# Optimization experiments

Hardware: AMD Instinct MI355X
Metric: run time of the kernel (lower is better)

The kernel has to match this reference:

```python
import jax, jax.numpy as jnp
import numpy as np
import math

B, T, C, H, E = 1, 384, 512, 8, 16
D = C // H

def layer_norm(x, w, b, eps=1e-5):
    mu = jnp.mean(x, axis=-1, keepdims=True)
    var = jnp.mean(jnp.square(x - mu), axis=-1, keepdims=True)
    return (x - mu) * jax.lax.rsqrt(var + eps) * w + b

def setup_inputs() -> dict:
    key = jax.random.key(0)
    ks = jax.random.split(key, 12)
    s = 0.02
    return {
        'x': jax.random.normal(ks[0], (B, T, C), jnp.float32),
        'bias_matrix': jax.random.randint(ks[1], (B, T, T), 0, E, jnp.int32),
        'ln1_w': jnp.ones((C,), jnp.float32),
        'ln1_b': jnp.zeros((C,), jnp.float32),
        'w_attn_w': jax.random.normal(ks[2], (3 * C, C), jnp.float32) * s,
        'w_attn_b': jnp.zeros((3 * C,), jnp.float32),
        'w_proj_w': jax.random.normal(ks[3], (C, C), jnp.float32) * s,
        'w_proj_b': jnp.zeros((C,), jnp.float32),
        'attn_bias_emb': jax.random.normal(ks[4], (E, H), jnp.float32) * s,
        'edge_emb': jax.random.normal(ks[5], (E, C), jnp.float32) * s,
        'w_edge_k_w': jax.random.normal(ks[6], (C, C), jnp.float32) * s,
        'w_edge_k_b': jnp.zeros((C,), jnp.float32),
        'w_edge_v_w': jax.random.normal(ks[7], (C, C), jnp.float32) * s,
        'w_edge_v_b': jnp.zeros((C,), jnp.float32),
        'ln2_w': jnp.ones((C,), jnp.float32),
        'ln2_b': jnp.zeros((C,), jnp.float32),
        'c_fc_w': jax.random.normal(ks[8], (4 * C, C), jnp.float32) * s,
        'c_fc_b': jnp.zeros((4 * C,), jnp.float32),
        'c_proj_w': jax.random.normal(ks[9], (C, 4 * C), jnp.float32) * s,
        'c_proj_b': jnp.zeros((C,), jnp.float32),
    }

def reference(x, bias_matrix, ln1_w, ln1_b, w_attn_w, w_attn_b, w_proj_w, w_proj_b,
              attn_bias_emb, edge_emb, w_edge_k_w, w_edge_k_b, w_edge_v_w, w_edge_v_b,
              ln2_w, ln2_b, c_fc_w, c_fc_b, c_proj_w, c_proj_b):
    # --- attention branch ---
    h = layer_norm(x, ln1_w, ln1_b)
    qkv = h @ w_attn_w.T + w_attn_b                      # (B,T,3C)
    q, k, v = jnp.split(qkv, 3, axis=-1)
    q = q.reshape(B, T, H, D).transpose(0, 2, 1, 3)      # (B,H,T,D)
    k = k.reshape(B, T, H, D).transpose(0, 2, 1, 3)
    v = v.reshape(B, T, H, D).transpose(0, 2, 1, 3)
    scale = math.sqrt(D)

    ee = edge_emb[bias_matrix]                           # (B,T,T,C)
    e_k = (ee @ w_edge_k_w.T + w_edge_k_b).reshape(B, T, T, H, D)
    # score[b,h,i,j] = sum_d q[b,h,i,d] * k[b,h,j,d] * e_k[b,i,j,h,d]
    scores = jnp.einsum('bhid,bhjd,bijhd->bhij', q, k, e_k) / scale

    mask = jnp.tril(jnp.ones((T, T), bool))              # causal, diag included
    scores = jnp.where(mask, scores, -jnp.inf)
    ab = attn_bias_emb[bias_matrix].transpose(0, 3, 1, 2)  # (B,H,T,T)
    ab = jnp.where(mask, ab, 0.0)
    attn = jax.nn.softmax(scores + ab, axis=-1)

    e_v = (ee @ w_edge_v_w.T + w_edge_v_b).reshape(B, T, T, H, D)
    # y[b,h,i,d] = sum_j attn[b,h,i,j] * v[b,h,j,d] * e_v[b,i,j,h,d]
    y = jnp.einsum('bhij,bhjd,bijhd->bhid', attn, v, e_v)
    y = y.transpose(0, 2, 1, 3).reshape(B, T, C)
    y = y @ w_proj_w.T + w_proj_b
    x = x + y

    # --- MLP branch ---
    h2 = layer_norm(x, ln2_w, ln2_b)
    h2 = jax.nn.gelu(h2 @ c_fc_w.T + c_fc_b, approximate=False)
    x = x + (h2 @ c_proj_w.T + c_proj_b)
    return x
```

## Files before the change

kernel.cpp:

```cpp
#include <hip/hip_runtime.h>
#include <math.h>

#define TT 384
#define CC 512
#define HH 8
#define EE 16

typedef __bf16 bf16_t;
typedef __bf16 bf16x8 __attribute__((ext_vector_type(8)));
typedef __bf16 bf16x4v __attribute__((ext_vector_type(4)));
typedef float f32x4 __attribute__((ext_vector_type(4)));

__device__ __forceinline__ float wave_reduce_sum(float v) {
#pragma unroll
  for (int off = 32; off >= 1; off >>= 1) v += __shfl_xor(v, off, 64);
  return v;
}

__device__ __forceinline__ void wrow_unit(const float* __restrict__ wr,
                                          const float* __restrict__ g,
                                          const float* __restrict__ bb,
                                          float extra_c, bf16_t* __restrict__ orow,
                                          float* __restrict__ s1p,
                                          float* __restrict__ cp, int lane) {
  const float* p = wr + lane * 8;
  f32x4 w0 = *(const f32x4*)p, w1 = *(const f32x4*)(p + 4);
  f32x4 g0 = *(const f32x4*)(g + lane * 8), g1 = *(const f32x4*)(g + lane * 8 + 4);
  f32x4 b0 = *(const f32x4*)(bb + lane * 8), b1 = *(const f32x4*)(bb + lane * 8 + 4);
  f32x4 p0 = w0 * g0, p1 = w1 * g1;
  bf16x8 o;
  o[0] = (bf16_t)p0.x; o[1] = (bf16_t)p0.y; o[2] = (bf16_t)p0.z; o[3] = (bf16_t)p0.w;
  o[4] = (bf16_t)p1.x; o[5] = (bf16_t)p1.y; o[6] = (bf16_t)p1.z; o[7] = (bf16_t)p1.w;
  *(bf16x8*)(orow + lane * 8) = o;
  float s1 = p0.x + p0.y + p0.z + p0.w + p1.x + p1.y + p1.z + p1.w;
  float c = w0.x * b0.x + w0.y * b0.y + w0.z * b0.z + w0.w * b0.w +
            w1.x * b1.x + w1.y * b1.y + w1.z * b1.z + w1.w * b1.w;
  s1 = wave_reduce_sum(s1);
  c = wave_reduce_sum(c);
  if (lane == 0) { *s1p = s1; *cp = c + extra_c; }
}

struct PrepX {
  const float *eemb, *wekw, *wekb, *wevw, *wevb;
  const float *ln2w, *ln2b, *cfcw, *cfcb;
  const float *wproj, *wcproj;
  float *ektab, *evtab, *s1f, *cf, *x1s1, *x1s2;
  bf16_t *wfc_bf, *wproj_bf, *wcproj_bf;
};

__device__ void prep_unit(int u, const PrepX& X, int tid) {
  int lane = tid & 63, wave = tid >> 6;
  if (u < 256) {
    int wid = u * 4 + wave;
    int gbase = wid * 16;
    int table = gbase >> 13;
    int e = (gbase >> 9) & 15;
    int c0 = gbase & 511;
    const float* er = X.eemb + e * 512 + lane * 8;
    f32x4 ea = *(const f32x4*)er;
    f32x4 eb = *(const f32x4*)(er + 4);
    const float* wbase = table ? X.wevw : X.wekw;
    const float* bbase = table ? X.wevb : X.wekb;
    float* obase = (table ? X.evtab : X.ektab) + e * 512;
#pragma unroll
    for (int o = 0; o < 16; o++) {
      int c = c0 + o;
      const float* wr = wbase + (size_t)c * 512 + lane * 8;
      f32x4 wa = *(const f32x4*)wr;
      f32x4 wb = *(const f32x4*)(wr + 4);
      float acc = ea.x * wa.x + ea.y * wa.y + ea.z * wa.z + ea.w * wa.w +
                  eb.x * wb.x + eb.y * wb.y + eb.z * wb.z + eb.w * wb.w;
      acc = wave_reduce_sum(acc);
      if (lane == 0) obase[c] = acc + bbase[c];
    }
  } else if (u < 768) {
    int n = (u - 256) * 4 + wave;
    wrow_unit(X.cfcw + (size_t)n * 512, X.ln2w, X.ln2b, X.cfcb[n],
              X.wfc_bf + (size_t)n * 512, X.s1f + n, X.cf + n, lane);
  } else if (u < 1024) {
    int base = (u - 768) * 1024;
    for (int t = tid; t < 1024; t += 256) {
      f32x4 a = *((const f32x4*)X.wcproj + base + t);
      bf16x4v o;
      o[0] = (bf16_t)a.x; o[1] = (bf16_t)a.y; o[2] = (bf16_t)a.z; o[3] = (bf16_t)a.w;
      *((bf16x4v*)X.wcproj_bf + base + t) = o;
    }
  } else if (u < 1088) {
    int base = (u - 1024) * 1024;
    for (int t = tid; t < 1024; t += 256) {
      f32x4 a = *((const f32x4*)X.wproj + base + t);
      bf16x4v o;
      o[0] = (bf16_t)a.x; o[1] = (bf16_t)a.y; o[2] = (bf16_t)a.z; o[3] = (bf16_t)a.w;
      *((bf16x4v*)X.wproj_bf + base + t) = o;
    }
  } else if (u == 1088) {
    for (int i = tid; i < 384; i += 256) { X.x1s1[i] = 0.f; X.x1s2[i] = 0.f; }
  }
}

__global__ __launch_bounds__(256) void qkv_k(
    const float* __restrict__ x, const float* __restrict__ wattn,
    const float* __restrict__ ln1w, const float* __restrict__ ln1b,
    const float* __restrict__ wattnb, bf16_t* __restrict__ out, PrepX X) {
  int tid = threadIdx.x;
  if (blockIdx.y >= 12) {
    prep_unit((blockIdx.y - 12) * gridDim.x + blockIdx.x, X, tid);
    return;
  }
  __shared__ float part[4][32][32];
  __shared__ float rst[2][4][32];
  __shared__ float wst[2][4][32];
  int lane = tid & 63, wave = tid >> 6;
  int m0 = blockIdx.y * 32, n0 = blockIdx.x * 32;
  int r16 = lane & 15, quad = lane >> 4;
  int k0 = wave * 128;

  f32x4 acc[2][2];
  f32x4 zero = {0.f, 0.f, 0.f, 0.f};
#pragma unroll
  for (int i = 0; i < 2; i++)
#pragma unroll
    for (int j = 0; j < 2; j++) acc[i][j] = zero;

  const float* Af = x + (size_t)(m0 + r16) * 512 + k0 + quad * 8;
  const float* Wf = wattn + (size_t)(n0 + r16) * 512 + k0 + quad * 8;
  const float* gp = ln1w + k0 + quad * 8;
  const float* bp = ln1b + k0 + quad * 8;

  float sx[2] = {0.f, 0.f}, sxx[2] = {0.f, 0.f};
  float s1[2] = {0.f, 0.f}, cc[2] = {0.f, 0.f};

  for (int kb0 = 0; kb0 < 128; kb0 += 64) {
    uint4 araw[2][2][2], wraw[2][2][2];
#pragma unroll
    for (int u = 0; u < 2; u++) {
      int kb = kb0 + u * 32;
#pragma unroll
      for (int t = 0; t < 2; t++) {
        araw[u][t][0] = *(const uint4*)(Af + (size_t)t * 16 * 512 + kb);
        araw[u][t][1] = *(const uint4*)(Af + (size_t)t * 16 * 512 + kb + 4);
        wraw[u][t][0] = *(const uint4*)(Wf + (size_t)t * 16 * 512 + kb);
        wraw[u][t][1] = *(const uint4*)(Wf + (size_t)t * 16 * 512 + kb + 4);
      }
    }
#pragma unroll
    for (int u = 0; u < 2; u++) {
      int kb = kb0 + u * 32;
      f32x4 g0 = *(const f32x4*)(gp + kb), g1 = *(const f32x4*)(gp + kb + 4);
      f32x4 b0 = *(const f32x4*)(bp + kb), b1 = *(const f32x4*)(bp + kb + 4);
      bf16x8 af[2], bfr[2];
#pragma unroll
      for (int t = 0; t < 2; t++) {
        f32x4 a0 = *reinterpret_cast<const f32x4*>(&araw[u][t][0]);
        f32x4 a1 = *reinterpret_cast<const f32x4*>(&araw[u][t][1]);
        af[t][0] = (bf16_t)a0.x; af[t][1] = (bf16_t)a0.y;
        af[t][2] = (bf16_t)a0.z; af[t][3] = (bf16_t)a0.w;
        af[t][4] = (bf16_t)a1.x; af[t][5] = (bf16_t)a1.y;
        af[t][6] = (bf16_t)a1.z; af[t][7] = (bf16_t)a1.w;
        sx[t] += a0.x + a0.y + a0.z + a0.w + a1.x + a1.y + a1.z + a1.w;
        sxx[t] += a0.x * a0.x + a0.y * a0.y + a0.z * a0.z + a0.w * a0.w +
                  a1.x * a1.x + a1.y * a1.y + a1.z * a1.z + a1.w * a1.w;
        f32x4 w0 = *reinterpret_cast<const f32x4*>(&wraw[u][t][0]);
        f32x4 w1 = *reinterpret_cast<const f32x4*>(&wraw[u][t][1]);
        f32x4 p0 = w0 * g0, p1 = w1 * g1;
        bfr[t][0] = (bf16_t)p0.x; bfr[t][1] = (bf16_t)p0.y;
        bfr[t][2] = (bf16_t)p0.z; bfr[t][3] = (bf16_t)p0.w;
        bfr[t][4] = (bf16_t)p1.x; bfr[t][5] = (bf16_t)p1.y;
        bfr[t][6] = (bf16_t)p1.z; bfr[t][7] = (bf16_t)p1.w;
        s1[t] += p0.x + p0.y + p0.z + p0.w + p1.x + p1.y + p1.z + p1.w;
        cc[t] += w0.x * b0.x + w0.y * b0.y + w0.z * b0.z + w0.w * b0.w +
                 w1.x * b1.x + w1.y * b1.y + w1.z * b1.z + w1.w * b1.w;
      }
#pragma unroll
      for (int i = 0; i < 2; i++)
#pragma unroll
        for (int j = 0; j < 2; j++)
          acc[i][j] = __builtin_amdgcn_mfma_f32_16x16x32_bf16(af[i], bfr[j],
                                                              acc[i][j], 0, 0, 0);
    }
  }

#pragma unroll
  for (int t = 0; t < 2; t++) {
    sx[t] += __shfl_xor(sx[t], 16, 64);  sx[t] += __shfl_xor(sx[t], 32, 64);
    sxx[t] += __shfl_xor(sxx[t], 16, 64); sxx[t] += __shfl_xor(sxx[t], 32, 64);
    s1[t] += __shfl_xor(s1[t], 16, 64);  s1[t] += __shfl_xor(s1[t], 32, 64);
    cc[t] += __shfl_xor(cc[t], 16, 64);  cc[t] += __shfl_xor(cc[t], 32, 64);
  }
  if (quad == 0) {
#pragma unroll
    for (int t = 0; t < 2; t++) {
      rst[0][wave][t * 16 + r16] = sx[t];
      rst[1][wave][t * 16 + r16] = sxx[t];
      wst[0][wave][t * 16 + r16] = s1[t];
      wst[1][wave][t * 16 + r16] = cc[t];
    }
  }
#pragma unroll
  for (int i = 0; i < 2; i++)
#pragma unroll
    for (int j = 0; j < 2; j++)
#pragma unroll
      for (int r = 0; r < 4; r++)
        part[wave][i * 16 + quad * 4 + r][j * 16 + r16] = acc[i][j][r];
  __syncthreads();

  int row = tid >> 3, c4 = (tid & 7) * 4;
  f32x4 v = *(const f32x4*)&part[0][row][c4];
  v += *(const f32x4*)&part[1][row][c4];
  v += *(const f32x4*)&part[2][row][c4];
  v += *(const f32x4*)&part[3][row][c4];
  float sxt = rst[0][0][row] + rst[0][1][row] + rst[0][2][row] + rst[0][3][row];
  float sxxt = rst[1][0][row] + rst[1][1][row] + rst[1][2][row] + rst[1][3][row];
  float mu = sxt * (1.0f / 512.0f);
  float var = sxxt * (1.0f / 512.0f) - mu * mu;
  float rs = rsqrtf(var + 1e-5f);
  int grow = m0 + row, gcol = n0 + c4;
  bf16x4v o;
#pragma unroll
  for (int t = 0; t < 4; t++) {
    int cl = c4 + t;
    float s1v = wst[0][0][cl] + wst[0][1][cl] + wst[0][2][cl] + wst[0][3][cl];
    float ccv = wst[1][0][cl] + wst[1][1][cl] + wst[1][2][cl] + wst[1][3][cl] +
                wattnb[n0 + cl];
    o[t] = (bf16_t)(rs * (v[t] - mu * s1v) + ccv);
  }
  *(bf16x4v*)(out + (size_t)grow * 1536 + gcol) = o;
}

template <int MODE>
__global__ __launch_bounds__(256) void gemm_k(
    const void* __restrict__ Aptr, const bf16_t* __restrict__ Wb,
    const float* __restrict__ e0, const float* __restrict__ e1,
    const float* __restrict__ e2, const float* __restrict__ e3,
    const float* __restrict__ res, void* __restrict__ out,
    float* __restrict__ st1, float* __restrict__ st2, int N, int K) {
  constexpr bool AF32 = (MODE == 2);
  constexpr int AW = AF32 ? 2 : 1;
  __shared__ float part[4][32][32];
  int tid = threadIdx.x;
  int lane = tid & 63, wave = tid >> 6;
  int m0 = blockIdx.y * 32, n0 = blockIdx.x * 32;
  int r16 = lane & 15, quad = lane >> 4;
  int kchunk = K >> 2, k0 = wave * kchunk;

  f32x4 acc[2][2];
  f32x4 zero = {0.f, 0.f, 0.f, 0.f};
#pragma unroll
  for (int i = 0; i < 2; i++)
#pragma unroll
    for (int j = 0; j < 2; j++) acc[i][j] = zero;

  const float* Af = (const float*)Aptr + (size_t)(m0 + r16) * K + k0 + quad * 8;
  const bf16_t* Ab = (const bf16_t*)Aptr + (size_t)(m0 + r16) * K + k0 + quad * 8;
  const bf16_t* Wp = Wb + (size_t)(n0 + r16) * K + k0 + quad * 8;

  for (int kb0 = 0; kb0 < kchunk; kb0 += 128) {
    uint4 araw[4][2][AW];
    uint4 braw[4][2];
#pragma unroll
    for (int u = 0; u < 4; u++) {
      int kb = kb0 + u * 32;
#pragma unroll
      for (int t = 0; t < 2; t++) {
        if (AF32) {
          araw[u][t][0] = *(const uint4*)(Af + (size_t)t * 16 * K + kb);
          araw[u][t][1] = *(const uint4*)(Af + (size_t)t * 16 * K + kb + 4);
        } else {
          araw[u][t][0] = *(const uint4*)(Ab + (size_t)t * 16 * K + kb);
        }
        braw[u][t] = *(const uint4*)(Wp + (size_t)t * 16 * K + kb);
      }
    }
#pragma unroll
    for (int u = 0; u < 4; u++) {
      bf16x8 af[2], bfr[2];
#pragma unroll
      for (int t = 0; t < 2; t++) {
        if (AF32) {
          f32x4 a = *reinterpret_cast<const f32x4*>(&araw[u][t][0]);
          f32x4 c = *reinterpret_cast<const f32x4*>(&araw[u][t][1]);
          af[t][0] = (bf16_t)a.x; af[t][1] = (bf16_t)a.y;
          af[t][2] = (bf16_t)a.z; af[t][3] = (bf16_t)a.w;
          af[t][4] = (bf16_t)c.x; af[t][5] = (bf16_t)c.y;
          af[t][6] = (bf16_t)c.z; af[t][7] = (bf16_t)c.w;
        } else {
          af[t] = *reinterpret_cast<const bf16x8*>(&araw[u][t][0]);
        }
        bfr[t] = *reinterpret_cast<const bf16x8*>(&braw[u][t]);
      }
#pragma unroll
      for (int i = 0; i < 2; i++)
#pragma unroll
        for (int j = 0; j < 2; j++)
          acc[i][j] = __builtin_amdgcn_mfma_f32_16x16x32_bf16(af[i], bfr[j],
                                                              acc[i][j], 0, 0, 0);
    }
  }

#pragma unroll
  for (int i = 0; i < 2; i++)
#pragma unroll
    for (int j = 0; j < 2; j++)
#pragma unroll
      for (int r = 0; r < 4; r++)
        part[wave][i * 16 + quad * 4 + r][j * 16 + r16] = acc[i][j][r];
  __syncthreads();

  int row = tid >> 3, c4 = (tid & 7) * 4;
  f32x4 v = *(const f32x4*)&part[0][row][c4];
  v += *(const f32x4*)&part[1][row][c4];
  v += *(const f32x4*)&part[2][row][c4];
  v += *(const f32x4*)&part[3][row][c4];
  int grow = m0 + row, gcol = n0 + c4;

  if (MODE == 2) {
    float S = e0[grow], Q = e1[grow];
    float mu = S * (1.0f / 512.0f);
    float var = Q * (1.0f / 512.0f) - mu * mu;
    float rs = rsqrtf(var + 1e-5f);
    f32x4 s1v = *(const f32x4*)(e2 + gcol);
    f32x4 ccv = *(const f32x4*)(e3 + gcol);
    bf16x4v o;
#pragma unroll
    for (int t = 0; t < 4; t++) {
      float xg = rs * (v[t] - mu * s1v[t]) + ccv[t];
      xg = 0.5f * xg * (1.0f + erff(xg * 0.70710678118654752f));
      o[t] = (bf16_t)xg;
    }
    *(bf16x4v*)((bf16_t*)out + (size_t)grow * N + gcol) = o;
  } else {
    v += *(const f32x4*)(e2 + gcol);
    v += *(const f32x4*)(res + (size_t)grow * N + gcol);
    *(f32x4*)((float*)out + (size_t)grow * N + gcol) = v;
    if (MODE == 1) {
      float sv = v.x + v.y + v.z + v.w;
      float qv = v.x * v.x + v.y * v.y + v.z * v.z + v.w * v.w;
      sv += __shfl_down(sv, 4, 8); qv += __shfl_down(qv, 4, 8);
      sv += __shfl_down(sv, 2, 8); qv += __shfl_down(qv, 2, 8);
      sv += __shfl_down(sv, 1, 8); qv += __shfl_down(qv, 1, 8);
      if ((tid & 7) == 0) {
        atomicAdd(st1 + grow, sv);
        atomicAdd(st2 + grow, qv);
      }
    }
  }
}

__global__ __launch_bounds__(256) void attn_k(
    const bf16_t* __restrict__ qkv, const int* __restrict__ bias_matrix,
    const float* __restrict__ attn_bias_emb, const float* __restrict__ ek_tab,
    const float* __restrict__ ev_tab, bf16_t* __restrict__ ybuf) {
  __shared__ uint2 ps1[TT], ps2[TT];
  __shared__ float qe1[EE][68], qe2[EE][68];
  __shared__ float evh[EE * 64];
  __shared__ float red[2][4 * 64];
  __shared__ float absh[EE];
  __shared__ float scr[2][4];

  int b = blockIdx.x, h = blockIdx.y;
  int i1 = b, i2 = (TT - 1) - b;
  int n1 = i1 + 1, n2 = i2 + 1;
  int tid = threadIdx.x, lane = tid & 63, wave = tid >> 6;

  if (tid < EE) absh[tid] = attn_bias_emb[tid * HH + h];
  for (int idx = tid; idx < EE * 64; idx += 256) {
    int e = idx >> 6, d = idx & 63;
    float q1 = (float)qkv[(size_t)i1 * 1536 + h * 64 + d];
    float q2 = (float)qkv[(size_t)i2 * 1536 + h * 64 + d];
    float ek = ek_tab[e * 512 + h * 64 + d];
    qe1[e][d] = q1 * ek;
    qe2[e][d] = q2 * ek;
    evh[idx] = ev_tab[e * 512 + h * 64 + d];
  }
  __syncthreads();

  float ls1 = 0.0f, ls2 = 0.0f;
  const int* bm1 = bias_matrix + (size_t)i1 * TT;
  const int* bm2 = bias_matrix + (size_t)i2 * TT;
  for (int jl = tid; jl < n2; jl += 256) {
    int e2 = bm2[jl];
    const uint4* kp = (const uint4*)(qkv + (size_t)jl * 1536 + 512 + h * 64);
    uint4 kr[8];
#pragma unroll
    for (int dg = 0; dg < 8; dg++) kr[dg] = kp[dg];
    float a2 = 0.f;
#pragma unroll
    for (int dg = 0; dg < 8; dg++) {
      bf16x8 kv = *reinterpret_cast<const bf16x8*>(&kr[dg]);
      f32x4 qa = *(const f32x4*)&qe2[e2][dg * 8];
      f32x4 qb = *(const f32x4*)&qe2[e2][dg * 8 + 4];
      a2 += (float)kv[0] * qa.x + (float)kv[1] * qa.y + (float)kv[2] * qa.z +
            (float)kv[3] * qa.w + (float)kv[4] * qb.x + (float)kv[5] * qb.y +
            (float)kv[6] * qb.z + (float)kv[7] * qb.w;
    }
    float p2 = __expf(a2 * 0.125f + absh[e2]);
    uint2 pk2; pk2.x = (unsigned)e2; pk2.y = __float_as_uint(p2);
    ps2[jl] = pk2;
    ls2 += p2;
    if (jl < n1) {
      int e1 = bm1[jl];
      float a1 = 0.f;
#pragma unroll
      for (int dg = 0; dg < 8; dg++) {
        bf16x8 kv = *reinterpret_cast<const bf16x8*>(&kr[dg]);
        f32x4 qa = *(const f32x4*)&qe1[e1][dg * 8];
        f32x4 qb = *(const f32x4*)&qe1[e1][dg * 8 + 4];
        a1 += (float)kv[0] * qa.x + (float)kv[1] * qa.y + (float)kv[2] * qa.z +
              (float)kv[3] * qa.w + (float)kv[4] * qb.x + (float)kv[5] * qb.y +
              (float)kv[6] * qb.z + (float)kv[7] * qb.w;
      }
      float p1 = __expf(a1 * 0.125f + absh[e1]);
      uint2 pk1; pk1.x = (unsigned)e1; pk1.y = __float_as_uint(p1);
      ps1[jl] = pk1;
      ls1 += p1;
    }
  }
  ls1 = wave_reduce_sum(ls1);
  ls2 = wave_reduce_sum(ls2);
  if (lane == 0) { scr[0][wave] = ls1; scr[1][wave] = ls2; }
  __syncthreads();
  float inv1 = 1.0f / (scr[0][0] + scr[0][1] + scr[0][2] + scr[0][3]);
  float inv2 = 1.0f / (scr[1][0] + scr[1][1] + scr[1][2] + scr[1][3]);

  const bf16_t* vb = qkv + 1024 + h * 64 + lane;
  float acc1 = 0.0f, acc2 = 0.0f;
  int j = wave;
  for (; j + 12 < n1; j += 16) {
    float v0 = (float)vb[(size_t)j * 1536];
    float v1 = (float)vb[(size_t)(j + 4) * 1536];
    float v2 = (float)vb[(size_t)(j + 8) * 1536];
    float v3 = (float)vb[(size_t)(j + 12) * 1536];
    uint2 c0 = ps2[j], c1 = ps2[j + 4], c2 = ps2[j + 8], c3 = ps2[j + 12];
    uint2 d0 = ps1[j], d1 = ps1[j + 4], d2 = ps1[j + 8], d3 = ps1[j + 12];
    acc2 = fmaf(__uint_as_float(c0.y) * v0, evh[c0.x * 64 + lane], acc2);
    acc2 = fmaf(__uint_as_float(c1.y) * v1, evh[c1.x * 64 + lane], acc2);
    acc2 = fmaf(__uint_as_float(c2.y) * v2, evh[c2.x * 64 + lane], acc2);
    acc2 = fmaf(__uint_as_float(c3.y) * v3, evh[c3.x * 64 + lane], acc2);
    acc1 = fmaf(__uint_as_float(d0.y) * v0, evh[d0.x * 64 + lane], acc1);
    acc1 = fmaf(__uint_as_float(d1.y) * v1, evh[d1.x * 64 + lane], acc1);
    acc1 = fmaf(__uint_as_float(d2.y) * v2, evh[d2.x * 64 + lane], acc1);
    acc1 = fmaf(__uint_as_float(d3.y) * v3, evh[d3.x * 64 + lane], acc1);
  }
  for (; j < n1; j += 4) {
    float v0 = (float)vb[(size_t)j * 1536];
    uint2 c0 = ps2[j], d0 = ps1[j];
    acc2 = fmaf(__uint_as_float(c0.y) * v0, evh[c0.x * 64 + lane], acc2);
    acc1 = fmaf(__uint_as_float(d0.y) * v0, evh[d0.x * 64 + lane], acc1);
  }
  for (; j + 12 < n2; j += 16) {
    float v0 = (float)vb[(size_t)j * 1536];
    float v1 = (float)vb[(size_t)(j + 4) * 1536];
    float v2 = (float)vb[(size_t)(j + 8) * 1536];
    float v3 = (float)vb[(size_t)(j + 12) * 1536];
    uint2 c0 = ps2[j], c1 = ps2[j + 4], c2 = ps2[j + 8], c3 = ps2[j + 12];
    acc2 = fmaf(__uint_as_float(c0.y) * v0, evh[c0.x * 64 + lane], acc2);
    acc2 = fmaf(__uint_as_float(c1.y) * v1, evh[c1.x * 64 + lane], acc2);
    acc2 = fmaf(__uint_as_float(c2.y) * v2, evh[c2.x * 64 + lane], acc2);
    acc2 = fmaf(__uint_as_float(c3.y) * v3, evh[c3.x * 64 + lane], acc2);
  }
  for (; j < n2; j += 4) {
    float v0 = (float)vb[(size_t)j * 1536];
    uint2 c0 = ps2[j];
    acc2 = fmaf(__uint_as_float(c0.y) * v0, evh[c0.x * 64 + lane], acc2);
  }
  red[0][wave * 64 + lane] = acc1;
  red[1][wave * 64 + lane] = acc2;
  __syncthreads();
  if (tid < 64) {
    float y =
        (red[0][tid] + red[0][64 + tid] + red[0][128 + tid] + red[0][192 + tid]) *
        inv1;
    ybuf[(size_t)i1 * CC + h * 64 + tid] = (bf16_t)y;
  } else if (tid < 128) {
    int t = tid - 64;
    float y =
        (red[1][t] + red[1][64 + t] + red[1][128 + t] + red[1][192 + t]) * inv2;
    ybuf[(size_t)i2 * CC + h * 64 + t] = (bf16_t)y;
  }
}

extern "C" void kernel_launch(void* const* d_in, const int* in_sizes, int n_in,
                              void* d_out, int out_size, void* d_ws,
                              size_t ws_size, hipStream_t stream) {
  const float* x = (const float*)d_in[0];
  const int* bias_mat = (const int*)d_in[1];

  char* wp = (char*)d_ws;
  float* ektab = (float*)wp;  wp += 16 * 512 * 4;
  float* evtab = (float*)wp;  wp += 16 * 512 * 4;
  float* x1s1 = (float*)wp;   wp += 384 * 4;
  float* x1s2 = (float*)wp;   wp += 384 * 4;
  float* s1f = (float*)wp;    wp += 2048 * 4;
  float* cf = (float*)wp;     wp += 2048 * 4;
  float* x1 = (float*)wp;     wp += 384 * 512 * 4;
  bf16_t* wfc_bf = (bf16_t*)wp;    wp += 2048 * 512 * 2;
  bf16_t* wproj_bf = (bf16_t*)wp;  wp += 512 * 512 * 2;
  bf16_t* wcproj_bf = (bf16_t*)wp; wp += 512 * 2048 * 2;
  bf16_t* qkv = (bf16_t*)wp;  wp += 384 * 1536 * 2;
  bf16_t* ybuf = (bf16_t*)wp; wp += 384 * 512 * 2;
  bf16_t* gbuf = (bf16_t*)wp; wp += 384 * 2048 * 2;

  PrepX X;
  X.eemb = (const float*)d_in[9];
  X.wekw = (const float*)d_in[10];
  X.wekb = (const float*)d_in[11];
  X.wevw = (const float*)d_in[12];
  X.wevb = (const float*)d_in[13];
  X.ln2w = (const float*)d_in[14];
  X.ln2b = (const float*)d_in[15];
  X.cfcw = (const float*)d_in[16];
  X.cfcb = (const float*)d_in[17];
  X.wproj = (const float*)d_in[6];
  X.wcproj = (const float*)d_in[18];
  X.ektab = ektab; X.evtab = evtab; X.s1f = s1f; X.cf = cf;
  X.x1s1 = x1s1; X.x1s2 = x1s2;
  X.wfc_bf = wfc_bf; X.wproj_bf = wproj_bf; X.wcproj_bf = wcproj_bf;

  qkv_k<<<dim3(48, 35), 256, 0, stream>>>(
      x, (const float*)d_in[4], (const float*)d_in[2], (const float*)d_in[3],
      (const float*)d_in[5], qkv, X);
  attn_k<<<dim3(TT / 2, HH), 256, 0, stream>>>(qkv, bias_mat,
                                               (const float*)d_in[8], ektab,
                                               evtab, ybuf);
  gemm_k<1><<<dim3(16, 12), 256, 0, stream>>>(
      ybuf, wproj_bf, nullptr, nullptr, (const float*)d_in[7], nullptr, x, x1,
      x1s1, x1s2, 512, 512);
  gemm_k<2><<<dim3(64, 12), 256, 0, stream>>>(x1, wfc_bf, x1s1, x1s2, s1f, cf,
                                              nullptr, gbuf, nullptr, nullptr,
                                              2048, 512);
  gemm_k<3><<<dim3(16, 12), 256, 0, stream>>>(
      gbuf, wcproj_bf, nullptr, nullptr, (const float*)d_in[19], nullptr, x1,
      d_out, nullptr, nullptr, 512, 2048);
}
```

Measured before the change: 167.3 us.

## Fuse output projection GEMM into attention kernel via per-tile completion counters

The attention kernel now ends with a per-row-tile atomic counter. The block that finishes the last of the 256 contributions to a 32-row tile computes that tile's output projection, residual add and LayerNorm row statistics, so the separate projection GEMM launch is removed. This aims to cut one kernel launch and the round-trip of ybuf through a new grid. The cost is that each tile's 32x512 projection now runs serially inside one block on only 12 tiles, which may add tail latency. It also reuses attention shared memory through a union.

```diff
diff --git a/kernel.cpp b/kernel.cpp
--- a/kernel.cpp
+++ b/kernel.cpp
@@ -46,6 +46,7 @@
   const float *wproj, *wcproj;
   float *ektab, *evtab, *s1f, *cf, *x1s1, *x1s2;
   bf16_t *wfc_bf, *wproj_bf, *wcproj_bf;
+  int *cnt;
 };
 
 __device__ void prep_unit(int u, const PrepX& X, int tid) {
@@ -95,6 +96,7 @@
     }
   } else if (u == 1088) {
     for (int i = tid; i < 384; i += 256) { X.x1s1[i] = 0.f; X.x1s2[i] = 0.f; }
+    if (tid < 12) X.cnt[tid] = 0;
   }
 }
 
@@ -333,30 +335,35 @@
     v += *(const f32x4*)(e2 + gcol);
     v += *(const f32x4*)(res + (size_t)grow * N + gcol);
     *(f32x4*)((float*)out + (size_t)grow * N + gcol) = v;
-    if (MODE == 1) {
-      float sv = v.x + v.y + v.z + v.w;
-      float qv = v.x * v.x + v.y * v.y + v.z * v.z + v.w * v.w;
-      sv += __shfl_down(sv, 4, 8); qv += __shfl_down(qv, 4, 8);
-      sv += __shfl_down(sv, 2, 8); qv += __shfl_down(qv, 2, 8);
-      sv += __shfl_down(sv, 1, 8); qv += __shfl_down(qv, 1, 8);
-      if ((tid & 7) == 0) {
-        atomicAdd(st1 + grow, sv);
-        atomicAdd(st2 + grow, qv);
-      }
-    }
   }
 }
 
 __global__ __launch_bounds__(256) void attn_k(
     const bf16_t* __restrict__ qkv, const int* __restrict__ bias_matrix,
     const float* __restrict__ attn_bias_emb, const float* __restrict__ ek_tab,
-    const float* __restrict__ ev_tab, bf16_t* __restrict__ ybuf) {
-  __shared__ uint2 ps1[TT], ps2[TT];
-  __shared__ float qe1[EE][68], qe2[EE][68];
-  __shared__ float evh[EE * 64];
+    const float* __restrict__ ev_tab, bf16_t* __restrict__ ybuf,
+    const bf16_t* __restrict__ wproj_bf, const float* __restrict__ wprojb,
+    const float* __restrict__ x, float* __restrict__ x1,
+    float* __restrict__ x1s1, float* __restrict__ x1s2,
+    int* __restrict__ cnt) {
+  __shared__ union {
+    struct {
+      uint2 ps1[TT], ps2[TT];
+      float qe1[EE][68], qe2[EE][68];
+      float evh[EE * 64];
+    } a;
+    float part[4][32][32];
+  } U;
   __shared__ float red[2][4 * 64];
   __shared__ float absh[EE];
   __shared__ float scr[2][4];
+  __shared__ int exec_t[2];
+
+  uint2* ps1 = U.a.ps1;
+  uint2* ps2 = U.a.ps2;
+  float(*qe1)[68] = U.a.qe1;
+  float(*qe2)[68] = U.a.qe2;
+  float* evh = U.a.evh;
 
   int b = blockIdx.x, h = blockIdx.y;
   int i1 = b, i2 = (TT - 1) - b;
@@ -478,6 +485,96 @@
         (red[1][t] + red[1][64 + t] + red[1][128 + t] + red[1][192 + t]) * inv2;
     ybuf[(size_t)i2 * CC + h * 64 + t] = (bf16_t)y;
   }
+
+  __threadfence();
+  __syncthreads();
+  if (tid == 0) {
+    int t1 = i1 >> 5, t2 = i2 >> 5;
+    int p1 = __hip_atomic_fetch_add(cnt + t1, 1, __ATOMIC_ACQ_REL,
+                                    __HIP_MEMORY_SCOPE_AGENT);
+    int p2 = __hip_atomic_fetch_add(cnt + t2, 1, __ATOMIC_ACQ_REL,
+                                    __HIP_MEMORY_SCOPE_AGENT);
+    exec_t[0] = (p1 == 255) ? t1 : -1;
+    exec_t[1] = (p2 == 255) ? t2 : -1;
+  }
+  __syncthreads();
+
+#pragma unroll 1
+  for (int s = 0; s < 2; s++) {
+    int tt = exec_t[s];
+    if (tt < 0) continue;
+    int m0 = tt * 32;
+    int r16 = lane & 15, quad = lane >> 4;
+    int k0 = wave * 128;
+    uint4 areg[4][2];
+    const bf16_t* Ab = ybuf + (size_t)(m0 + r16) * 512 + k0 + quad * 8;
+#pragma unroll
+    for (int u = 0; u < 4; u++)
+#pragma unroll
+      for (int t = 0; t < 2; t++)
+        areg[u][t] = *(const uint4*)(Ab + (size_t)t * 16 * 512 + u * 32);
+#pragma unroll 1
+    for (int bx = 0; bx < 16; bx++) {
+      int n0 = bx * 32;
+      const bf16_t* Wp = wproj_bf + (size_t)(n0 + r16) * 512 + k0 + quad * 8;
+      uint4 braw[4][2];
+#pragma unroll
+      for (int u = 0; u < 4; u++)
+#pragma unroll
+        for (int t = 0; t < 2; t++)
+          braw[u][t] = *(const uint4*)(Wp + (size_t)t * 16 * 512 + u * 32);
+      f32x4 acc[2][2];
+      f32x4 zero = {0.f, 0.f, 0.f, 0.f};
+#pragma unroll
+      for (int i = 0; i < 2; i++)
+#pragma unroll
+        for (int jj = 0; jj < 2; jj++) acc[i][jj] = zero;
+#pragma unroll
+      for (int u = 0; u < 4; u++) {
+        bf16x8 af[2], bfr[2];
+#pragma unroll
+        for (int t = 0; t < 2; t++) {
+          af[t] = *reinterpret_cast<const bf16x8*>(&areg[u][t]);
+          bfr[t] = *reinterpret_cast<const bf16x8*>(&braw[u][t]);
+        }
+#pragma unroll
+        for (int i = 0; i < 2; i++)
+#pragma unroll
+          for (int jj = 0; jj < 2; jj++)
+            acc[i][jj] = __builtin_amdgcn_mfma_f32_16x16x32_bf16(
+                af[i], bfr[jj], acc[i][jj], 0, 0, 0);
+      }
+#pragma unroll
+      for (int i = 0; i < 2; i++)
+#pragma unroll
+        for (int jj = 0; jj < 2; jj++)
+#pragma unroll
+          for (int r = 0; r < 4; r++)
+            U.part[wave][i * 16 + quad * 4 + r][jj * 16 + r16] = acc[i][jj][r];
+      __syncthreads();
+      {
+        int row = tid >> 3, c4 = (tid & 7) * 4;
+        f32x4 v = *(const f32x4*)&U.part[0][row][c4];
+        v += *(const f32x4*)&U.part[1][row][c4];
+        v += *(const f32x4*)&U.part[2][row][c4];
+        v += *(const f32x4*)&U.part[3][row][c4];
+        int grow = m0 + row, gcol = n0 + c4;
+        v += *(const f32x4*)(wprojb + gcol);
+        v += *(const f32x4*)(x + (size_t)grow * 512 + gcol);
+        *(f32x4*)(x1 + (size_t)grow * 512 + gcol) = v;
+        float sv = v.x + v.y + v.z + v.w;
+        float qv = v.x * v.x + v.y * v.y + v.z * v.z + v.w * v.w;
+        sv += __shfl_down(sv, 4, 8); qv += __shfl_down(qv, 4, 8);
+        sv += __shfl_down(sv, 2, 8); qv += __shfl_down(qv, 2, 8);
+        sv += __shfl_down(sv, 1, 8); qv += __shfl_down(qv, 1, 8);
+        if ((tid & 7) == 0) {
+          atomicAdd(x1s1 + grow, sv);
+          atomicAdd(x1s2 + grow, qv);
+        }
+      }
+      __syncthreads();
+    }
+  }
 }
 
 extern "C" void kernel_launch(void* const* d_in, const int* in_sizes, int n_in,
@@ -500,6 +597,7 @@
   bf16_t* qkv = (bf16_t*)wp;  wp += 384 * 1536 * 2;
   bf16_t* ybuf = (bf16_t*)wp; wp += 384 * 512 * 2;
   bf16_t* gbuf = (bf16_t*)wp; wp += 384 * 2048 * 2;
+  int* cnt = (int*)wp;        wp += 16 * 4;
 
   PrepX X;
   X.eemb = (const float*)d_in[9];
@@ -516,16 +614,14 @@
   X.ektab = ektab; X.evtab = evtab; X.s1f = s1f; X.cf = cf;
   X.x1s1 = x1s1; X.x1s2 = x1s2;
   X.wfc_bf = wfc_bf; X.wproj_bf = wproj_bf; X.wcproj_bf = wcproj_bf;
+  X.cnt = cnt;
 
   qkv_k<<<dim3(48, 35), 256, 0, stream>>>(
       x, (const float*)d_in[4], (const float*)d_in[2], (const float*)d_in[3],
       (const float*)d_in[5], qkv, X);
-  attn_k<<<dim3(TT / 2, HH), 256, 0, stream>>>(qkv, bias_mat,
-                                               (const float*)d_in[8], ektab,
-                                               evtab, ybuf);
-  gemm_k<1><<<dim3(16, 12), 256, 0, stream>>>(
-      ybuf, wproj_bf, nullptr, nullptr, (const float*)d_in[7], nullptr, x, x1,
-      x1s1, x1s2, 512, 512);
+  attn_k<<<dim3(TT / 2, HH), 256, 0, stream>>>(
+      qkv, bias_mat, (const float*)d_in[8], ektab, evtab, ybuf, wproj_bf,
+      (const float*)d_in[7], x, x1, x1s1, x1s2, cnt);
   gemm_k<2><<<dim3(64, 12), 256, 0, stream>>>(x1, wfc_bf, x1s1, x1s2, s1f, cf,
                                               nullptr, gbuf, nullptr, nullptr,
                                               2048, 512);
```

Result: slower. 373.6 us (+123.4%).

## Compute LN2 row stats inside FC GEMM and pack attention probs into uint4

Applied to the files above, without the earlier changes.

Removes the atomicAdd-based row sum and sum-of-squares accumulation from the output-projection GEMM, along with the zeroing pass in the prep kernel. The FC GEMM now computes these LN2 statistics itself from the fp32 A tiles it already loads, reducing them across lanes and waves through shared memory. Separately, the attention kernel packs both rows' (edge index, prob) pairs into one uint4 shared array, so the shared loop reads them with one wide load. This trades global atomics for redundant per-block stat computation across 64 column blocks.

```diff
diff --git a/kernel.cpp b/kernel.cpp
--- a/kernel.cpp
+++ b/kernel.cpp
@@ -44,7 +44,7 @@
   const float *eemb, *wekw, *wekb, *wevw, *wevb;
   const float *ln2w, *ln2b, *cfcw, *cfcb;
   const float *wproj, *wcproj;
-  float *ektab, *evtab, *s1f, *cf, *x1s1, *x1s2;
+  float *ektab, *evtab, *s1f, *cf;
   bf16_t *wfc_bf, *wproj_bf, *wcproj_bf;
 };
 
@@ -93,8 +93,6 @@
       o[0] = (bf16_t)a.x; o[1] = (bf16_t)a.y; o[2] = (bf16_t)a.z; o[3] = (bf16_t)a.w;
       *((bf16x4v*)X.wproj_bf + base + t) = o;
     }
-  } else if (u == 1088) {
-    for (int i = tid; i < 384; i += 256) { X.x1s1[i] = 0.f; X.x1s2[i] = 0.f; }
   }
 }
 
@@ -231,13 +229,12 @@
 template <int MODE>
 __global__ __launch_bounds__(256) void gemm_k(
     const void* __restrict__ Aptr, const bf16_t* __restrict__ Wb,
-    const float* __restrict__ e0, const float* __restrict__ e1,
     const float* __restrict__ e2, const float* __restrict__ e3,
-    const float* __restrict__ res, void* __restrict__ out,
-    float* __restrict__ st1, float* __restrict__ st2, int N, int K) {
+    const float* __restrict__ res, void* __restrict__ out, int N, int K) {
   constexpr bool AF32 = (MODE == 2);
   constexpr int AW = AF32 ? 2 : 1;
   __shared__ float part[4][32][32];
+  __shared__ float rst[2][4][32];
   int tid = threadIdx.x;
   int lane = tid & 63, wave = tid >> 6;
   int m0 = blockIdx.y * 32, n0 = blockIdx.x * 32;
@@ -254,6 +251,8 @@
   const float* Af = (const float*)Aptr + (size_t)(m0 + r16) * K + k0 + quad * 8;
   const bf16_t* Ab = (const bf16_t*)Aptr + (size_t)(m0 + r16) * K + k0 + quad * 8;
   const bf16_t* Wp = Wb + (size_t)(n0 + r16) * K + k0 + quad * 8;
+
+  float sx[2] = {0.f, 0.f}, sxx[2] = {0.f, 0.f};
 
   for (int kb0 = 0; kb0 < kchunk; kb0 += 128) {
     uint4 araw[4][2][AW];
@@ -284,6 +283,9 @@
           af[t][2] = (bf16_t)a.z; af[t][3] = (bf16_t)a.w;
           af[t][4] = (bf16_t)c.x; af[t][5] = (bf16_t)c.y;
           af[t][6] = (bf16_t)c.z; af[t][7] = (bf16_t)c.w;
+          sx[t] += a.x + a.y + a.z + a.w + c.x + c.y + c.z + c.w;
+          sxx[t] += a.x * a.x + a.y * a.y + a.z * a.z + a.w * a.w +
+                    c.x * c.x + c.y * c.y + c.z * c.z + c.w * c.w;
         } else {
           af[t] = *reinterpret_cast<const bf16x8*>(&araw[u][t][0]);
         }
@@ -298,6 +300,20 @@
     }
   }
 
+  if (MODE == 2) {
+#pragma unroll
+    for (int t = 0; t < 2; t++) {
+      sx[t] += __shfl_xor(sx[t], 16, 64);  sx[t] += __shfl_xor(sx[t], 32, 64);
+      sxx[t] += __shfl_xor(sxx[t], 16, 64); sxx[t] += __shfl_xor(sxx[t], 32, 64);
+    }
+    if (quad == 0) {
+#pragma unroll
+      for (int t = 0; t < 2; t++) {
+        rst[0][wave][t * 16 + r16] = sx[t];
+        rst[1][wave][t * 16 + r16] = sxx[t];
+      }
+    }
+  }
 #pragma unroll
   for (int i = 0; i < 2; i++)
 #pragma unroll
@@ -315,7 +331,8 @@
   int grow = m0 + row, gcol = n0 + c4;
 
   if (MODE == 2) {
-    float S = e0[grow], Q = e1[grow];
+    float S = rst[0][0][row] + rst[0][1][row] + rst[0][2][row] + rst[0][3][row];
+    float Q = rst[1][0][row] + rst[1][1][row] + rst[1][2][row] + rst[1][3][row];
     float mu = S * (1.0f / 512.0f);
     float var = Q * (1.0f / 512.0f) - mu * mu;
     float rs = rsqrtf(var + 1e-5f);
@@ -333,17 +350,6 @@
     v += *(const f32x4*)(e2 + gcol);
     v += *(const f32x4*)(res + (size_t)grow * N + gcol);
     *(f32x4*)((float*)out + (size_t)grow * N + gcol) = v;
-    if (MODE == 1) {
-      float sv = v.x + v.y + v.z + v.w;
-      float qv = v.x * v.x + v.y * v.y + v.z * v.z + v.w * v.w;
-      sv += __shfl_down(sv, 4, 8); qv += __shfl_down(qv, 4, 8);
-      sv += __shfl_down(sv, 2, 8); qv += __shfl_down(qv, 2, 8);
-      sv += __shfl_down(sv, 1, 8); qv += __shfl_down(qv, 1, 8);
-      if ((tid & 7) == 0) {
-        atomicAdd(st1 + grow, sv);
-        atomicAdd(st2 + grow, qv);
-      }
-    }
   }
 }
 
@@ -351,7 +357,7 @@
     const bf16_t* __restrict__ qkv, const int* __restrict__ bias_matrix,
     const float* __restrict__ attn_bias_emb, const float* __restrict__ ek_tab,
     const float* __restrict__ ev_tab, bf16_t* __restrict__ ybuf) {
-  __shared__ uint2 ps1[TT], ps2[TT];
+  __shared__ uint4 psv[TT];
   __shared__ float qe1[EE][68], qe2[EE][68];
   __shared__ float evh[EE * 64];
   __shared__ float red[2][4 * 64];
@@ -395,8 +401,9 @@
             (float)kv[6] * qb.z + (float)kv[7] * qb.w;
     }
     float p2 = __expf(a2 * 0.125f + absh[e2]);
-    uint2 pk2; pk2.x = (unsigned)e2; pk2.y = __float_as_uint(p2);
-    ps2[jl] = pk2;
+    uint4 pk;
+    pk.x = 0u; pk.y = 0u;
+    pk.z = (unsigned)e2; pk.w = __float_as_uint(p2);
     ls2 += p2;
     if (jl < n1) {
       int e1 = bm1[jl];
@@ -411,10 +418,11 @@
               (float)kv[6] * qb.z + (float)kv[7] * qb.w;
       }
       float p1 = __expf(a1 * 0.125f + absh[e1]);
-      uint2 pk1; pk1.x = (unsigned)e1; pk1.y = __float_as_uint(p1);
-      ps1[jl] = pk1;
+      pk.x = (unsigned)e1;
+      pk.y = __float_as_uint(p1);
       ls1 += p1;
     }
+    psv[jl] = pk;
   }
   ls1 = wave_reduce_sum(ls1);
   ls2 = wave_reduce_sum(ls2);
@@ -431,29 +439,30 @@
     float v1 = (float)vb[(size_t)(j + 4) * 1536];
     float v2 = (float)vb[(size_t)(j + 8) * 1536];
     float v3 = (float)vb[(size_t)(j + 12) * 1536];
-    uint2 c0 = ps2[j], c1 = ps2[j + 4], c2 = ps2[j + 8], c3 = ps2[j + 12];
-    uint2 d0 = ps1[j], d1 = ps1[j + 4], d2 = ps1[j + 8], d3 = ps1[j + 12];
-    acc2 = fmaf(__uint_as_float(c0.y) * v0, evh[c0.x * 64 + lane], acc2);
-    acc2 = fmaf(__uint_as_float(c1.y) * v1, evh[c1.x * 64 + lane], acc2);
-    acc2 = fmaf(__uint_as_float(c2.y) * v2, evh[c2.x * 64 + lane], acc2);
-    acc2 = fmaf(__uint_as_float(c3.y) * v3, evh[c3.x * 64 + lane], acc2);
-    acc1 = fmaf(__uint_as_float(d0.y) * v0, evh[d0.x * 64 + lane], acc1);
-    acc1 = fmaf(__uint_as_float(d1.y) * v1, evh[d1.x * 64 + lane], acc1);
-    acc1 = fmaf(__uint_as_float(d2.y) * v2, evh[d2.x * 64 + lane], acc1);
-    acc1 = fmaf(__uint_as_float(d3.y) * v3, evh[d3.x * 64 + lane], acc1);
+    uint4 q0 = psv[j], q1 = psv[j + 4], q2 = psv[j + 8], q3 = psv[j + 12];
+    acc2 = fmaf(__uint_as_float(q0.w) * v0, evh[q0.z * 64 + lane], acc2);
+    acc2 = fmaf(__uint_as_float(q1.w) * v1, evh[q1.z * 64 + lane], acc2);
+    acc2 = fmaf(__uint_as_float(q2.w) * v2, evh[q2.z * 64 + lane], acc2);
+    acc2 = fmaf(__uint_as_float(q3.w) * v3, evh[q3.z * 64 + lane], acc2);
+    acc1 = fmaf(__uint_as_float(q0.y) * v0, evh[q0.x * 64 + lane], acc1);
+    acc1 = fmaf(__uint_as_float(q1.y) * v1, evh[q1.x * 64 + lane], acc1);
+    acc1 = fmaf(__uint_as_float(q2.y) * v2, evh[q2.x * 64 + lane], acc1);
+    acc1 = fmaf(__uint_as_float(q3.y) * v3, evh[q3.x * 64 + lane], acc1);
   }
   for (; j < n1; j += 4) {
     float v0 = (float)vb[(size_t)j * 1536];
-    uint2 c0 = ps2[j], d0 = ps1[j];
-    acc2 = fmaf(__uint_as_float(c0.y) * v0, evh[c0.x * 64 + lane], acc2);
-    acc1 = fmaf(__uint_as_float(d0.y) * v0, evh[d0.x * 64 + lane], acc1);
-  }
+    uint4 q0 = psv[j];
+    acc2 = fmaf(__uint_as_float(q0.w) * v0, evh[q0.z * 64 + lane], acc2);
+    acc1 = fmaf(__uint_as_float(q0.y) * v0, evh[q0.x * 64 + lane], acc1);
+  }
+  const uint2* ps2h = (const uint2*)((const char*)psv + 8);
   for (; j + 12 < n2; j += 16) {
     float v0 = (float)vb[(size_t)j * 1536];
     float v1 = (float)vb[(size_t)(j + 4) * 1536];
     float v2 = (float)vb[(size_t)(j + 8) * 1536];
     float v3 = (float)vb[(size_t)(j + 12) * 1536];
-    uint2 c0 = ps2[j], c1 = ps2[j + 4], c2 = ps2[j + 8], c3 = ps2[j + 12];
+    uint2 c0 = ps2h[j * 2], c1 = ps2h[(j + 4) * 2];
+    uint2 c2 = ps2h[(j + 8) * 2], c3 = ps2h[(j + 12) * 2];
     acc2 = fmaf(__uint_as_float(c0.y) * v0, evh[c0.x * 64 + lane], acc2);
     acc2 = fmaf(__uint_as_float(c1.y) * v1, evh[c1.x * 64 + lane], acc2);
     acc2 = fmaf(__uint_as_float(c2.y) * v2, evh[c2.x * 64 + lane], acc2);
@@ -461,7 +470,7 @@
   }
   for (; j < n2; j += 4) {
     float v0 = (float)vb[(size_t)j * 1536];
-    uint2 c0 = ps2[j];
+    uint2 c0 = ps2h[j * 2];
     acc2 = fmaf(__uint_as_float(c0.y) * v0, evh[c0.x * 64 + lane], acc2);
   }
   red[0][wave * 64 + lane] = acc1;
@@ -489,8 +498,6 @@
   char* wp = (char*)d_ws;
   float* ektab = (float*)wp;  wp += 16 * 512 * 4;
   float* evtab = (float*)wp;  wp += 16 * 512 * 4;
-  float* x1s1 = (float*)wp;   wp += 384 * 4;
-  float* x1s2 = (float*)wp;   wp += 384 * 4;
   float* s1f = (float*)wp;    wp += 2048 * 4;
   float* cf = (float*)wp;     wp += 2048 * 4;
   float* x1 = (float*)wp;     wp += 384 * 512 * 4;
@@ -514,7 +521,6 @@
   X.wproj = (const float*)d_in[6];
   X.wcproj = (const float*)d_in[18];
   X.ektab = ektab; X.evtab = evtab; X.s1f = s1f; X.cf = cf;
-  X.x1s1 = x1s1; X.x1s2 = x1s2;
   X.wfc_bf = wfc_bf; X.wproj_bf = wproj_bf; X.wcproj_bf = wcproj_bf;
 
   qkv_k<<<dim3(48, 35), 256, 0, stream>>>(
@@ -524,12 +530,9 @@
                                                (const float*)d_in[8], ektab,
                                                evtab, ybuf);
   gemm_k<1><<<dim3(16, 12), 256, 0, stream>>>(
-      ybuf, wproj_bf, nullptr, nullptr, (const float*)d_in[7], nullptr, x, x1,
-      x1s1, x1s2, 512, 512);
-  gemm_k<2><<<dim3(64, 12), 256, 0, stream>>>(x1, wfc_bf, x1s1, x1s2, s1f, cf,
-                                              nullptr, gbuf, nullptr, nullptr,
-                                              2048, 512);
+      ybuf, wproj_bf, (const float*)d_in[7], nullptr, x, x1, 512, 512);
+  gemm_k<2><<<dim3(64, 12), 256, 0, stream>>>(x1, wfc_bf, s1f, cf, nullptr,
+                                              gbuf, 2048, 512);
   gemm_k<3><<<dim3(16, 12), 256, 0, stream>>>(
-      gbuf, wcproj_bf, nullptr, nullptr, (const float*)d_in[19], nullptr, x1,
-      d_out, nullptr, nullptr, 512, 2048);
-}
+      gbuf, wcproj_bf, (const float*)d_in[19], nullptr, x1, d_out, 512, 2048);
+}
```

Result: no change. 167.9 us (+0.4%).
